# Optimization experiments

Measured on AMD Instinct MI355X. Metric: run time of the kernel, lower is better.

Reference implementation:

```python
import jax, jax.numpy as jnp
import numpy as np

N, E, H, NF, EF = 50000, 1600000, 128, 8, 2


def setup_inputs() -> dict:
    key = jax.random.key(0)
    ks = jax.random.split(key, 24)
    rn = lambda k, shp, s=0.05: jax.random.normal(k, shp, jnp.float32) * s
    inp = {
        "x": jax.random.normal(ks[0], (N, NF), jnp.float32),
        "edge_index": jax.random.randint(ks[1], (2, E), 0, N),
        "edge_attr": jax.random.normal(ks[2], (E, EF), jnp.float32),
        "enc_W": rn(ks[3], (NF, H)),
        "enc_b": jnp.zeros((H,), jnp.float32),
        "bn_g": jnp.ones((H,), jnp.float32),
        "bn_b": jnp.zeros((H,), jnp.float32),
    }
    i = 4
    for l in (1, 2, 3):
        inp[f"W{l}"] = rn(ks[i], (H, H))
        inp[f"asrc{l}"] = rn(ks[i + 1], (H,))
        inp[f"adst{l}"] = rn(ks[i + 2], (H,))
        inp[f"We{l}"] = rn(ks[i + 3], (EF, H))
        inp[f"ae{l}"] = rn(ks[i + 4], (H,))
        inp[f"b{l}"] = jnp.zeros((H,), jnp.float32)
        i += 5
    return inp


def _gat(h, src, dst, ea, W, a_s, a_d, We, a_e, b, n):
    # PyG GATConv, heads=1, concat=True, negative_slope=0.2
    g = h @ W                                   # [N, H] transformed nodes
    a_src = g @ a_s                             # [N] per-source attention term
    a_dst = g @ a_d                             # [N] per-target attention term
    a_edge = (ea @ We) @ a_e                    # [E'] edge-conditioned term
    logit = jax.nn.leaky_relu(a_src[src] + a_dst[dst] + a_edge, negative_slope=0.2)
    # scatter-softmax over incoming edges of each destination node
    m = jax.ops.segment_max(logit, dst, num_segments=n)
    e = jnp.exp(logit - m[dst])
    s = jax.ops.segment_sum(e, dst, num_segments=n)
    alpha = e / (s[dst] + 1e-16)                # [E']
    out = jax.ops.segment_sum(g[src] * alpha[:, None], dst, num_segments=n)
    return out + b


def _forward(x, edge_index, edge_attr, enc_W, enc_b, bn_g, bn_b,
             W1, asrc1, adst1, We1, ae1, b1,
             W2, asrc2, adst2, We2, ae2, b2,
             W3, asrc3, adst3, We3, ae3, b3):
    n = x.shape[0]
    # PyG add_self_loops=True with fill_value='mean' for edge_attr
    loop = jnp.arange(n)
    src = jnp.concatenate([edge_index[0], loop])
    dst = jnp.concatenate([edge_index[1], loop])
    ea = jnp.concatenate([edge_attr, jnp.broadcast_to(edge_attr.mean(0), (n, edge_attr.shape[1]))], axis=0)
    # node encoder: Linear -> BatchNorm1d (eval: running_mean=0, running_var=1) -> ReLU (dropout off)
    inv = np.float32(1.0 / np.sqrt(1.0 + 1e-5))
    h0 = jax.nn.relu((x @ enc_W + enc_b) * (bn_g * inv) + bn_b)
    h1 = jax.nn.relu(_gat(h0, src, dst, ea, W1, asrc1, adst1, We1, ae1, b1, n))
    h2 = jax.nn.relu(_gat(h1, src, dst, ea, W2, asrc2, adst2, We2, ae2, b2, n))
    h3 = _gat(h2, src, dst, ea, W3, asrc3, adst3, We3, ae3, b3, n)
    return h3 + h0


def reference(x, edge_index, edge_attr, enc_W, enc_b, bn_g, bn_b,
              W1, asrc1, adst1, We1, ae1, b1,
              W2, asrc2, adst2, We2, ae2, b2,
              W3, asrc3, adst3, We3, ae3, b3):
    return _forward(x, edge_index, edge_attr, enc_W, enc_b, bn_g, bn_b,
                    W1, asrc1, adst1, We1, ae1, b1,
                    W2, asrc2, adst2, We2, ae2, b2,
                    W3, asrc3, adst3, We3, ae3, b3)
```

## Files before the change

### kernel.cpp

```cpp
#include <hip/hip_runtime.h>
#include <math.h>


#define H 128
#define NF 8
#define EPB 4096

typedef __attribute__((ext_vector_type(8))) short short8v;
typedef __attribute__((ext_vector_type(4))) float f32x4;
typedef __attribute__((ext_vector_type(2))) float f32x2;

__device__ __forceinline__ float wred_sum(float x) {
#pragma unroll
    for (int m = 32; m >= 1; m >>= 1) x += __shfl_xor(x, m, 64);
    return x;
}
__device__ __forceinline__ float wred_max(float x) {
#pragma unroll
    for (int m = 32; m >= 1; m >>= 1) x = fmaxf(x, __shfl_xor(x, m, 64));
    return x;
}
__device__ __forceinline__ ushort f2bf(float f) {
    uint u = __float_as_uint(f);
    uint r = (u + 0x7FFFu + ((u >> 16) & 1u)) >> 16;
    return (ushort)r;
}
__device__ __forceinline__ f32x2 bfpair(uint q) {
    f32x2 r;
    r.x = __uint_as_float(q << 16);
    r.y = __uint_as_float(q & 0xffff0000u);
    return r;
}

__global__ void k_fusedA(const int* __restrict__ ei, const float* __restrict__ ea,
                         int E, int nblk, int nbuckets, int* __restrict__ bucketTotal,
                         int* __restrict__ blockBase, float2* __restrict__ pmean,
                         const float* __restrict__ x, const float* __restrict__ encW,
                         const float* __restrict__ encb, const float* __restrict__ bng,
                         const float* __restrict__ bnb, float* __restrict__ h0,
                         ushort* __restrict__ hb, int N, int GB8,
                         const float* __restrict__ W1, const float* __restrict__ W2,
                         const float* __restrict__ W3, ushort* __restrict__ Wp) {
    __shared__ int hist[256];
    __shared__ float sx[4], sy[4];
    __shared__ float xs[8 * NF];
    const int bx = blockIdx.x;
    const int t = threadIdx.x;

    if (bx < nblk) {
        int blk = bx;
        hist[t] = 0;
        __syncthreads();
        int base = blk * EPB;
        float px = 0.f, py = 0.f;
#pragma unroll
        for (int i = 0; i < 16; ++i) {
            int e = base + i * 256 + t;
            if (e < E) {
                int d = ei[E + e];
                atomicAdd(&hist[d >> 8], 1);
                const float2 z = *(const float2*)(ea + 2 * (size_t)e);
                px += z.x; py += z.y;
            }
        }
        px = wred_sum(px); py = wred_sum(py);
        if ((t & 63) == 0) { sx[t >> 6] = px; sy[t >> 6] = py; }
        __syncthreads();
        if (t == 0) {
            pmean[blk] = make_float2(sx[0] + sx[1] + sx[2] + sx[3],
                                     sy[0] + sy[1] + sy[2] + sy[3]);
        }
        if (t < nbuckets) {
            int c = hist[t];
            int old = (c > 0) ? atomicAdd(&bucketTotal[t], c) : 0;
            blockBase[t * nblk + blk] = old;
        }
    } else if (bx < nblk + GB8) {
        int nb = (bx - nblk) * 8;
        if (t < 64) {
            size_t idx = (size_t)nb * NF + t;
            xs[t] = (idx < (size_t)N * NF) ? x[idx] : 0.f;
        }
        __syncthreads();
        int jt = t & 31, i = t >> 5;
        int node = nb + i;
        int j4 = jt * 4;
        float ax = 0.f, ay = 0.f, az = 0.f, aw = 0.f;
#pragma unroll
        for (int k = 0; k < NF; ++k) {
            float hx = xs[i * NF + k];
            const float4 w = *(const float4*)(encW + k * H + j4);
            ax = fmaf(hx, w.x, ax); ay = fmaf(hx, w.y, ay);
            az = fmaf(hx, w.z, az); aw = fmaf(hx, w.w, aw);
        }
        if (node < N) {
            const float inv = 0.9999950000374997f;
            const float4 eb = *(const float4*)(encb + j4);
            const float4 gg = *(const float4*)(bng + j4);
            const float4 bb = *(const float4*)(bnb + j4);
            float4 o;
            o.x = fmaxf(0.f, (ax + eb.x) * (gg.x * inv) + bb.x);
            o.y = fmaxf(0.f, (ay + eb.y) * (gg.y * inv) + bb.y);
            o.z = fmaxf(0.f, (az + eb.z) * (gg.z * inv) + bb.z);
            o.w = fmaxf(0.f, (aw + eb.w) * (gg.w * inv) + bb.w);
            *(float4*)(h0 + (size_t)node * H + j4) = o;
            uint2 ob;
            ob.x = (uint)f2bf(o.x) | ((uint)f2bf(o.y) << 16);
            ob.y = (uint)f2bf(o.z) | ((uint)f2bf(o.w) << 16);
            *(uint2*)(hb + (size_t)node * H + j4) = ob;
        }
    } else {
        int layer = bx - nblk - GB8;
        const float* W = (layer == 0) ? W1 : ((layer == 1) ? W2 : W3);
        for (int idx = t; idx < 16384; idx += 256) {
            int i = idx & 7;
            int lane = (idx >> 3) & 63;
            int ft = idx >> 9;
            int kt = ft & 3, nt = ft >> 2;
            int k = kt * 32 + (lane >> 4) * 8 + i;
            int n = nt * 16 + (lane & 15);
            Wp[layer * 16384 + idx] = f2bf(W[k * H + n]);
        }
    }
}

__global__ void k_scan_park(const int* __restrict__ bucketTotal, int nbuckets,
                            int* __restrict__ bucketBase, int* __restrict__ rowptr,
                            int N, int E, const float2* __restrict__ pmean, int nblk,
                            float invE,
                            const float* __restrict__ We1, const float* __restrict__ ae1,
                            const float* __restrict__ We2, const float* __restrict__ ae2,
                            const float* __restrict__ We3, const float* __restrict__ ae3,
                            float* __restrict__ park) {
    __shared__ int tmp[256];
    __shared__ float2 sp[4];
    __shared__ float smean[2];
    int t = threadIdx.x;
    float ax = 0.f, ay = 0.f;
    for (int i = t; i < nblk; i += 256) {
        float2 z = pmean[i];
        ax += z.x; ay += z.y;
    }
    ax = wred_sum(ax); ay = wred_sum(ay);
    if ((t & 63) == 0) sp[t >> 6] = make_float2(ax, ay);
    int v = (t < nbuckets) ? bucketTotal[t] : 0;
    tmp[t] = v;
    __syncthreads();
    for (int off = 1; off < 256; off <<= 1) {
        int q = (t >= off) ? tmp[t - off] : 0;
        __syncthreads();
        tmp[t] += q;
        __syncthreads();
    }
    bucketBase[t] = tmp[t] - v;
    if (t == 0) {
        bucketBase[256] = tmp[255];
        rowptr[N] = E;
        smean[0] = (sp[0].x + sp[1].x + sp[2].x + sp[3].x) * invE;
        smean[1] = (sp[0].y + sp[1].y + sp[2].y + sp[3].y) * invE;
    }
    __syncthreads();
    if (t < 192) {
        int l = t >> 6, q = t & 63;
        const float* We = (l == 0) ? We1 : ((l == 1) ? We2 : We3);
        const float* ae = (l == 0) ? ae1 : ((l == 1) ? ae2 : ae3);
        float p0 = We[q] * ae[q] + We[q + 64] * ae[q + 64];
        float p1 = We[H + q] * ae[q] + We[H + q + 64] * ae[q + 64];
        p0 = wred_sum(p0);
        p1 = wred_sum(p1);
        if (q == 0) {
            park[l * 3 + 0] = p0;
            park[l * 3 + 1] = p1;
            park[l * 3 + 2] = smean[0] * p0 + smean[1] * p1;
        }
    }
}

__global__ void k_fusedB(const int* __restrict__ ei, const float* __restrict__ ea,
                         int E, int nblk, int nbuckets,
                         const int* __restrict__ bucketBase, const int* __restrict__ blockBase,
                         uint2* __restrict__ temp,
                         const ushort* __restrict__ hb, const ushort* __restrict__ Wp,
                         const float* __restrict__ avs, const float* __restrict__ avd,
                         ushort* __restrict__ gb, float* __restrict__ a_src,
                         float* __restrict__ a_dst, int N) {
    __shared__ int cnt[256];
    __shared__ int sbase[256];
    __shared__ ushort hs[64 * 136];
    const int tid = threadIdx.x;

    if (blockIdx.x < nblk) {
        int blk = blockIdx.x;
        cnt[tid] = 0;
        if (tid < nbuckets) sbase[tid] = bucketBase[tid] + blockBase[tid * nblk + blk];
        __syncthreads();
        int base = blk * EPB;
#pragma unroll
        for (int i = 0; i < 16; ++i) {
            int e = base + i * 256 + tid;
            if (e < E) {
                int s = ei[e];
                int d = ei[E + e];
                int b = d >> 8;
                int r = atomicAdd(&cnt[b], 1);
                const float2 z = *(const float2*)(ea + 2 * (size_t)e);
                uint w0 = (uint)s | ((uint)(d & 255) << 16);
                uint w1 = (uint)f2bf(z.x) | ((uint)f2bf(z.y) << 16);
                temp[sbase[b] + r] = make_uint2(w0, w1);
            }
        }
        return;
    }

    int nb = (blockIdx.x - nblk) * 64;
#pragma unroll
    for (int it = 0; it < 4; ++it) {
        int fi = it * 256 + tid;
        int r = fi >> 4;
        int c8 = (fi & 15) * 8;
        int node = nb + r;
        uint4 v = make_uint4(0, 0, 0, 0);
        if (node < N) v = *(const uint4*)(hb + (size_t)node * H + c8);
        *(uint4*)(hs + r * 136 + c8) = v;
    }
    __syncthreads();
    const int l = tid & 63;
    const int w = tid >> 6;
    const int cl = l & 15;
    const int kg = l >> 4;
    const ushort* hrow = hs + (w * 16 + cl) * 136 + kg * 8;
    short8v a0 = *(const short8v*)(hrow + 0);
    short8v a1 = *(const short8v*)(hrow + 32);
    short8v a2 = *(const short8v*)(hrow + 64);
    short8v a3 = *(const short8v*)(hrow + 96);

    f32x4 acc[8];
#pragma unroll
    for (int nt = 0; nt < 8; ++nt) {
        const short8v* bp = (const short8v*)(Wp + ((size_t)(nt * 4) * 64 + l) * 8);
        f32x4 c = {0.f, 0.f, 0.f, 0.f};
        c = __builtin_amdgcn_mfma_f32_16x16x32_bf16(a0, bp[0], c, 0, 0, 0);
        c = __builtin_amdgcn_mfma_f32_16x16x32_bf16(a1, bp[64], c, 0, 0, 0);
        c = __builtin_amdgcn_mfma_f32_16x16x32_bf16(a2, bp[128], c, 0, 0, 0);
        c = __builtin_amdgcn_mfma_f32_16x16x32_bf16(a3, bp[192], c, 0, 0, 0);
        acc[nt] = c;
    }

    float ps0 = 0.f, ps1 = 0.f, ps2 = 0.f, ps3 = 0.f;
    float pd0 = 0.f, pd1 = 0.f, pd2 = 0.f, pd3 = 0.f;
#pragma unroll
    for (int nt = 0; nt < 8; ++nt) {
        float vs = avs[cl + 16 * nt];
        float vd = avd[cl + 16 * nt];
        ps0 = fmaf(acc[nt].x, vs, ps0); pd0 = fmaf(acc[nt].x, vd, pd0);
        ps1 = fmaf(acc[nt].y, vs, ps1); pd1 = fmaf(acc[nt].y, vd, pd1);
        ps2 = fmaf(acc[nt].z, vs, ps2); pd2 = fmaf(acc[nt].z, vd, pd2);
        ps3 = fmaf(acc[nt].w, vs, ps3); pd3 = fmaf(acc[nt].w, vd, pd3);
    }
#pragma unroll
    for (int m = 8; m >= 1; m >>= 1) {
        ps0 += __shfl_xor(ps0, m, 64); pd0 += __shfl_xor(pd0, m, 64);
        ps1 += __shfl_xor(ps1, m, 64); pd1 += __shfl_xor(pd1, m, 64);
        ps2 += __shfl_xor(ps2, m, 64); pd2 += __shfl_xor(pd2, m, 64);
        ps3 += __shfl_xor(ps3, m, 64); pd3 += __shfl_xor(pd3, m, 64);
    }
    int r0 = nb + w * 16 + kg * 4;
    if (cl == 0) {
        if (r0 + 0 < N) { a_src[r0 + 0] = ps0; a_dst[r0 + 0] = pd0; }
        if (r0 + 1 < N) { a_src[r0 + 1] = ps1; a_dst[r0 + 1] = pd1; }
        if (r0 + 2 < N) { a_src[r0 + 2] = ps2; a_dst[r0 + 2] = pd2; }
        if (r0 + 3 < N) { a_src[r0 + 3] = ps3; a_dst[r0 + 3] = pd3; }
    }
#pragma unroll
    for (int nt = 0; nt < 8; ++nt) {
        int col = nt * 16 + cl;
        if (r0 + 0 < N) gb[(size_t)(r0 + 0) * H + col] = f2bf(acc[nt].x);
        if (r0 + 1 < N) gb[(size_t)(r0 + 1) * H + col] = f2bf(acc[nt].y);
        if (r0 + 2 < N) gb[(size_t)(r0 + 2) * H + col] = f2bf(acc[nt].z);
        if (r0 + 3 < N) gb[(size_t)(r0 + 3) * H + col] = f2bf(acc[nt].w);
    }
}

__global__ void k_fine(const uint2* __restrict__ temp, const int* __restrict__ bucketBase,
                       const float* __restrict__ park, int N,
                       uint* __restrict__ er0, uint* __restrict__ er1,
                       uint* __restrict__ er2, int* __restrict__ rowptr) {
    __shared__ int hist[256];
    __shared__ int tmp[256];
    __shared__ int fb[256];
    __shared__ int cur[256];
    int b = blockIdx.x;
    int t = threadIdx.x;
    const int lo = bucketBase[b], hi = bucketBase[b + 1];
    hist[t] = 0;
    __syncthreads();
    for (int e = lo + t; e < hi; e += 256) {
        atomicAdd(&hist[(temp[e].x >> 16) & 255], 1);
    }
    __syncthreads();
    int v = hist[t];
    tmp[t] = v;
    __syncthreads();
    for (int off = 1; off < 256; off <<= 1) {
        int q = (t >= off) ? tmp[t - off] : 0;
        __syncthreads();
        tmp[t] += q;
        __syncthreads();
    }
    fb[t] = tmp[t] - v;
    cur[t] = 0;
    int dst = b * 256 + t;
    if (dst < N) rowptr[dst] = lo + fb[t];
    __syncthreads();
    const float c00 = park[0], c01 = park[1];
    const float c10 = park[3], c11 = park[4];
    const float c20 = park[6], c21 = park[7];
    for (int e = lo + t; e < hi; e += 256) {
        uint2 w = temp[e];
        uint src = w.x & 0xFFFFu;
        int j = (int)((w.x >> 16) & 255u);
        float ex = __uint_as_float(w.y << 16);
        float ey = __uint_as_float(w.y & 0xffff0000u);
        int r = atomicAdd(&cur[j], 1);
        int p = lo + fb[j] + r;
        er0[p] = src | ((uint)f2bf(c00 * ex + c01 * ey) << 16);
        er1[p] = src | ((uint)f2bf(c10 * ex + c11 * ey) << 16);
        er2[p] = src | ((uint)f2bf(c20 * ex + c21 * ey) << 16);
    }
}

__global__ void k_gemm_mfma(const ushort* __restrict__ hb, const ushort* __restrict__ Wp,
                            const float* __restrict__ avs, const float* __restrict__ avd,
                            ushort* __restrict__ gb, float* __restrict__ a_src,
                            float* __restrict__ a_dst, int N) {
    __shared__ ushort hs[64 * 136];
    int tid = threadIdx.x;
    int nb = blockIdx.x * 64;
#pragma unroll
    for (int it = 0; it < 4; ++it) {
        int fi = it * 256 + tid;
        int r = fi >> 4;
        int c8 = (fi & 15) * 8;
        int node = nb + r;
        uint4 v = make_uint4(0, 0, 0, 0);
        if (node < N) v = *(const uint4*)(hb + (size_t)node * H + c8);
        *(uint4*)(hs + r * 136 + c8) = v;
    }
    __syncthreads();
    const int l = tid & 63;
    const int w = tid >> 6;
    const int cl = l & 15;
    const int kg = l >> 4;
    const ushort* hrow = hs + (w * 16 + cl) * 136 + kg * 8;
    short8v a0 = *(const short8v*)(hrow + 0);
    short8v a1 = *(const short8v*)(hrow + 32);
    short8v a2 = *(const short8v*)(hrow + 64);
    short8v a3 = *(const short8v*)(hrow + 96);

    f32x4 acc[8];
#pragma unroll
    for (int nt = 0; nt < 8; ++nt) {
        const short8v* bp = (const short8v*)(Wp + ((size_t)(nt * 4) * 64 + l) * 8);
        f32x4 c = {0.f, 0.f, 0.f, 0.f};
        c = __builtin_amdgcn_mfma_f32_16x16x32_bf16(a0, bp[0], c, 0, 0, 0);
        c = __builtin_amdgcn_mfma_f32_16x16x32_bf16(a1, bp[64], c, 0, 0, 0);
        c = __builtin_amdgcn_mfma_f32_16x16x32_bf16(a2, bp[128], c, 0, 0, 0);
        c = __builtin_amdgcn_mfma_f32_16x16x32_bf16(a3, bp[192], c, 0, 0, 0);
        acc[nt] = c;
    }

    float ps0 = 0.f, ps1 = 0.f, ps2 = 0.f, ps3 = 0.f;
    float pd0 = 0.f, pd1 = 0.f, pd2 = 0.f, pd3 = 0.f;
#pragma unroll
    for (int nt = 0; nt < 8; ++nt) {
        float vs = avs[cl + 16 * nt];
        float vd = avd[cl + 16 * nt];
        ps0 = fmaf(acc[nt].x, vs, ps0); pd0 = fmaf(acc[nt].x, vd, pd0);
        ps1 = fmaf(acc[nt].y, vs, ps1); pd1 = fmaf(acc[nt].y, vd, pd1);
        ps2 = fmaf(acc[nt].z, vs, ps2); pd2 = fmaf(acc[nt].z, vd, pd2);
        ps3 = fmaf(acc[nt].w, vs, ps3); pd3 = fmaf(acc[nt].w, vd, pd3);
    }
#pragma unroll
    for (int m = 8; m >= 1; m >>= 1) {
        ps0 += __shfl_xor(ps0, m, 64); pd0 += __shfl_xor(pd0, m, 64);
        ps1 += __shfl_xor(ps1, m, 64); pd1 += __shfl_xor(pd1, m, 64);
        ps2 += __shfl_xor(ps2, m, 64); pd2 += __shfl_xor(pd2, m, 64);
        ps3 += __shfl_xor(ps3, m, 64); pd3 += __shfl_xor(pd3, m, 64);
    }
    int r0 = nb + w * 16 + kg * 4;
    if (cl == 0) {
        if (r0 + 0 < N) { a_src[r0 + 0] = ps0; a_dst[r0 + 0] = pd0; }
        if (r0 + 1 < N) { a_src[r0 + 1] = ps1; a_dst[r0 + 1] = pd1; }
        if (r0 + 2 < N) { a_src[r0 + 2] = ps2; a_dst[r0 + 2] = pd2; }
        if (r0 + 3 < N) { a_src[r0 + 3] = ps3; a_dst[r0 + 3] = pd3; }
    }
#pragma unroll
    for (int nt = 0; nt < 8; ++nt) {
        int col = nt * 16 + cl;
        if (r0 + 0 < N) gb[(size_t)(r0 + 0) * H + col] = f2bf(acc[nt].x);
        if (r0 + 1 < N) gb[(size_t)(r0 + 1) * H + col] = f2bf(acc[nt].y);
        if (r0 + 2 < N) gb[(size_t)(r0 + 2) * H + col] = f2bf(acc[nt].z);
        if (r0 + 3 < N) gb[(size_t)(r0 + 3) * H + col] = f2bf(acc[nt].w);
    }
}

template <int MODE>
__global__ void k_agg(const ushort* __restrict__ gb, const float* __restrict__ a_src,
                      const float* __restrict__ a_dst, const int* __restrict__ rowptr,
                      const uint* __restrict__ erecL, const float* __restrict__ park,
                      int layer, const float* __restrict__ bias,
                      const float* __restrict__ h0, float* __restrict__ outf,
                      ushort* __restrict__ outb, int N) {
    int wv = threadIdx.x >> 6;
    int lane = threadIdx.x & 63;
    int v = blockIdx.x * 4 + wv;
    if (v >= N) return;

    const int grp = lane >> 4;
    const int sub = lane & 15;
    const int ch8 = sub * 8;

    const float sa = park[layer * 3 + 2];
    const float adv = a_dst[v];
    float lself = a_src[v] + adv + sa;
    lself = (lself > 0.f) ? lself : 0.2f * lself;

    float m = lself;
    float s = 1.f;
    f32x2 acc2[4];
    {
        const uint4 q = *(const uint4*)(gb + (size_t)v * H + ch8);
        float sel = (grp == 0) ? 1.f : 0.f;
        acc2[0] = bfpair(q.x) * sel;
        acc2[1] = bfpair(q.y) * sel;
        acc2[2] = bfpair(q.z) * sel;
        acc2[3] = bfpair(q.w) * sel;
    }

    const int rs = rowptr[v];
    const int re = rowptr[v + 1];
    for (int p0 = rs; p0 < re; p0 += 64) {
        int e = p0 + lane;
        bool val = e < re;
        uint rec = val ? __builtin_nontemporal_load(erecL + e) : 0u;
        int sv = (int)(rec & 0xFFFFu);
        float lg;
        if (val) {
            float aef = __uint_as_float(rec & 0xffff0000u);
            lg = a_src[sv] + adv + aef;
            lg = (lg > 0.f) ? lg : 0.2f * lg;
        } else {
            lg = -INFINITY;
        }
        float cm = wred_max(lg);
        float nm = fmaxf(m, cm);
        float f = __expf(m - nm);
        float w = val ? __expf(lg - nm) : 0.f;
        float ws = wred_sum(w);
        s = s * f + ws;
#pragma unroll
        for (int k = 0; k < 4; ++k) acc2[k] *= f;
        m = nm;

        int cnt = re - p0;
        if (cnt > 64) cnt = 64;
        const int cm1 = cnt - 1;
        const int iters = (cnt + 7) >> 3;

        int jA = grp, jB = grp + 4;
        int jAc = (jA <= cm1) ? jA : cm1;
        int jBc = (jB <= cm1) ? jB : cm1;
        float wA = __shfl(w, jAc, 64); if (jA > cm1) wA = 0.f;
        float wB = __shfl(w, jBc, 64); if (jB > cm1) wB = 0.f;
        int sA = __shfl(sv, jAc, 64);
        int sB = __shfl(sv, jBc, 64);
        uint4 qA = *(const uint4*)(gb + (size_t)sA * H + ch8);
        uint4 qB = *(const uint4*)(gb + (size_t)sB * H + ch8);

        for (int i = 0; i < iters; ++i) {
            int jA1 = (i + 1) * 8 + grp, jB1 = jA1 + 4;
            int jA1c = (jA1 <= cm1) ? jA1 : cm1;
            int jB1c = (jB1 <= cm1) ? jB1 : cm1;
            float wA1 = __shfl(w, jA1c, 64); if (jA1 > cm1) wA1 = 0.f;
            float wB1 = __shfl(w, jB1c, 64); if (jB1 > cm1) wB1 = 0.f;
            int sA1 = __shfl(sv, jA1c, 64);
            int sB1 = __shfl(sv, jB1c, 64);
            uint4 qA1 = *(const uint4*)(gb + (size_t)sA1 * H + ch8);
            uint4 qB1 = *(const uint4*)(gb + (size_t)sB1 * H + ch8);

            f32x2 wAv = {wA, wA};
            f32x2 wBv = {wB, wB};
            acc2[0] = __builtin_elementwise_fma(wAv, bfpair(qA.x), acc2[0]);
            acc2[1] = __builtin_elementwise_fma(wAv, bfpair(qA.y), acc2[1]);
            acc2[2] = __builtin_elementwise_fma(wAv, bfpair(qA.z), acc2[2]);
            acc2[3] = __builtin_elementwise_fma(wAv, bfpair(qA.w), acc2[3]);
            acc2[0] = __builtin_elementwise_fma(wBv, bfpair(qB.x), acc2[0]);
            acc2[1] = __builtin_elementwise_fma(wBv, bfpair(qB.y), acc2[1]);
            acc2[2] = __builtin_elementwise_fma(wBv, bfpair(qB.z), acc2[2]);
            acc2[3] = __builtin_elementwise_fma(wBv, bfpair(qB.w), acc2[3]);

            wA = wA1; wB = wB1; qA = qA1; qB = qB1;
        }
    }

    float acc[8];
    acc[0] = acc2[0].x; acc[1] = acc2[0].y;
    acc[2] = acc2[1].x; acc[3] = acc2[1].y;
    acc[4] = acc2[2].x; acc[5] = acc2[2].y;
    acc[6] = acc2[3].x; acc[7] = acc2[3].y;
#pragma unroll
    for (int k = 0; k < 8; ++k) {
        acc[k] += __shfl_xor(acc[k], 16, 64);
        acc[k] += __shfl_xor(acc[k], 32, 64);
    }

    if (grp == 0) {
        const float is = 1.f / s;
        const float4 b0 = *(const float4*)(bias + ch8);
        const float4 b1 = *(const float4*)(bias + ch8 + 4);
        float o[8];
        o[0] = acc[0] * is + b0.x; o[1] = acc[1] * is + b0.y;
        o[2] = acc[2] * is + b0.z; o[3] = acc[3] * is + b0.w;
        o[4] = acc[4] * is + b1.x; o[5] = acc[5] * is + b1.y;
        o[6] = acc[6] * is + b1.z; o[7] = acc[7] * is + b1.w;
        if (MODE == 0) {
#pragma unroll
            for (int k = 0; k < 8; ++k) o[k] = fmaxf(o[k], 0.f);
            uint4 ob;
            ob.x = (uint)f2bf(o[0]) | ((uint)f2bf(o[1]) << 16);
            ob.y = (uint)f2bf(o[2]) | ((uint)f2bf(o[3]) << 16);
            ob.z = (uint)f2bf(o[4]) | ((uint)f2bf(o[5]) << 16);
            ob.w = (uint)f2bf(o[6]) | ((uint)f2bf(o[7]) << 16);
            *(uint4*)(outb + (size_t)v * H + ch8) = ob;
        } else {
            const float4 ha = *(const float4*)(h0 + (size_t)v * H + ch8);
            const float4 hb4 = *(const float4*)(h0 + (size_t)v * H + ch8 + 4);
            o[0] += ha.x; o[1] += ha.y; o[2] += ha.z; o[3] += ha.w;
            o[4] += hb4.x; o[5] += hb4.y; o[6] += hb4.z; o[7] += hb4.w;
            *(float4*)(outf + (size_t)v * H + ch8) = make_float4(o[0], o[1], o[2], o[3]);
            *(float4*)(outf + (size_t)v * H + ch8 + 4) = make_float4(o[4], o[5], o[6], o[7]);
        }
    }
}


extern "C" void kernel_launch(void* const* d_in, const int* in_sizes, int n_in,
                              void* d_out, int out_size, void* d_ws, size_t ws_size,
                              hipStream_t stream) {
    const float* x    = (const float*)d_in[0];
    const int*   ei   = (const int*)d_in[1];
    const float* ea   = (const float*)d_in[2];
    const float* encW = (const float*)d_in[3];
    const float* encb = (const float*)d_in[4];
    const float* bng  = (const float*)d_in[5];
    const float* bnb  = (const float*)d_in[6];
    const float *W[3], *asrc[3], *adst[3], *We[3], *aev[3], *bias[3];
    for (int l = 0; l < 3; ++l) {
        W[l]    = (const float*)d_in[7 + l * 6 + 0];
        asrc[l] = (const float*)d_in[7 + l * 6 + 1];
        adst[l] = (const float*)d_in[7 + l * 6 + 2];
        We[l]   = (const float*)d_in[7 + l * 6 + 3];
        aev[l]  = (const float*)d_in[7 + l * 6 + 4];
        bias[l] = (const float*)d_in[7 + l * 6 + 5];
    }
    const int N = in_sizes[0] / NF;
    const int E = in_sizes[1] / 2;
    float* out = (float*)d_out;

    const int NBu  = (N + 255) >> 8;
    const int nblk = (E + EPB - 1) / EPB;
    const int GB8  = (N + 7) / 8;
    const int GBM  = (N + 63) / 64;
    const int AB   = (N + 3) / 4;

    char* wp = (char*)d_ws;
    auto alloc = [&](size_t bytes) -> char* {
        char* p = wp;
        wp += (bytes + 255) & ~(size_t)255;
        return p;
    };
    float*  h0       = (float*)alloc((size_t)N * H * 4);
    ushort* hb       = (ushort*)alloc((size_t)N * H * 2);
    ushort* gb       = (ushort*)alloc((size_t)N * H * 2);
    ushort* Wp       = (ushort*)alloc((size_t)3 * 16384 * 2);
    float*  a_src    = (float*)alloc((size_t)N * 4);
    float*  a_dst    = (float*)alloc((size_t)N * 4);
    int*    rowptr   = (int*)alloc((size_t)(N + 1) * 4);
    float*  park     = (float*)alloc(64);
    int*    bucketTotal = (int*)alloc(256 * 4);
    int*    bucketBase  = (int*)alloc(257 * 4);
    int*    blockBase   = (int*)alloc((size_t)NBu * nblk * 4);
    uint*   er0      = (uint*)alloc((size_t)E * 4);
    uint*   er1      = (uint*)alloc((size_t)E * 4);
    uint*   er2      = (uint*)alloc((size_t)E * 4);
    float2* pmean    = (float2*)alloc((size_t)nblk * 8);
    uint2*  temp     = (uint2*)alloc((size_t)E * 8);

    hipMemsetAsync(bucketTotal, 0, 256 * 4, stream);

    k_fusedA<<<nblk + GB8 + 3, 256, 0, stream>>>(
        ei, ea, E, nblk, NBu, bucketTotal, blockBase, pmean,
        x, encW, encb, bng, bnb, h0, hb, N, GB8,
        W[0], W[1], W[2], Wp);
    k_scan_park<<<1, 256, 0, stream>>>(bucketTotal, NBu, bucketBase, rowptr, N, E,
                                       pmean, nblk, 1.0f / (float)E,
                                       We[0], aev[0], We[1], aev[1], We[2], aev[2], park);
    k_fusedB<<<nblk + GBM, 256, 0, stream>>>(
        ei, ea, E, nblk, NBu, bucketBase, blockBase, temp,
        hb, Wp + 0 * 16384, asrc[0], adst[0], gb, a_src, a_dst, N);
    k_fine<<<NBu, 256, 0, stream>>>(temp, bucketBase, park, N, er0, er1, er2, rowptr);

    k_agg<0><<<AB, 256, 0, stream>>>(gb, a_src, a_dst, rowptr, er0, park, 0,
                                     bias[0], nullptr, nullptr, hb, N);
    k_gemm_mfma<<<GBM, 256, 0, stream>>>(hb, Wp + 1 * 16384, asrc[1], adst[1],
                                         gb, a_src, a_dst, N);
    k_agg<0><<<AB, 256, 0, stream>>>(gb, a_src, a_dst, rowptr, er1, park, 1,
                                     bias[1], nullptr, nullptr, hb, N);
    k_gemm_mfma<<<GBM, 256, 0, stream>>>(hb, Wp + 2 * 16384, asrc[2], adst[2],
                                         gb, a_src, a_dst, N);
    k_agg<1><<<AB, 256, 0, stream>>>(gb, a_src, a_dst, rowptr, er2, park, 2,
                                     bias[2], h0, out, nullptr, N);
}
```

Measured before the change: 298.8 us.

## Split aggregation into softmax-stats pass and channel-sliced gather pass

Replaces the single online-softmax aggregation kernel with two kernels: one computes each node's max and inverse softmax sum, and the other gathers neighbor features with exact weights. The gather is split into four 32-channel slices across separate blocks, with 16 edges handled in parallel per wave instead of 4 software-pipelined pairs. This removes the per-chunk rescaling and is meant to raise memory-level parallelism and occupancy in the gather. In exchange, the edge records, a_src lookups and exponentials are recomputed in both kernels and four times across the slices, and three extra launches are added.

```diff
diff --git a/kernel.cpp b/kernel.cpp
--- a/kernel.cpp
+++ b/kernel.cpp
@@ -8,7 +8,6 @@
 
 typedef __attribute__((ext_vector_type(8))) short short8v;
 typedef __attribute__((ext_vector_type(4))) float f32x4;
-typedef __attribute__((ext_vector_type(2))) float f32x2;
 
 __device__ __forceinline__ float wred_sum(float x) {
 #pragma unroll
@@ -25,12 +24,8 @@
     uint r = (u + 0x7FFFu + ((u >> 16) & 1u)) >> 16;
     return (ushort)r;
 }
-__device__ __forceinline__ f32x2 bfpair(uint q) {
-    f32x2 r;
-    r.x = __uint_as_float(q << 16);
-    r.y = __uint_as_float(q & 0xffff0000u);
-    return r;
-}
+__device__ __forceinline__ float bflo(uint q) { return __uint_as_float(q << 16); }
+__device__ __forceinline__ float bfhi(uint q) { return __uint_as_float(q & 0xffff0000u); }
 
 __global__ void k_fusedA(const int* __restrict__ ei, const float* __restrict__ ea,
                          int E, int nblk, int nbuckets, int* __restrict__ bucketTotal,
@@ -404,22 +399,15 @@
     }
 }
 
-template <int MODE>
-__global__ void k_agg(const ushort* __restrict__ gb, const float* __restrict__ a_src,
-                      const float* __restrict__ a_dst, const int* __restrict__ rowptr,
-                      const uint* __restrict__ erecL, const float* __restrict__ park,
-                      int layer, const float* __restrict__ bias,
-                      const float* __restrict__ h0, float* __restrict__ outf,
-                      ushort* __restrict__ outb, int N) {
+__global__ void k_soft(const float* __restrict__ a_src, const float* __restrict__ a_dst,
+                       const int* __restrict__ rowptr, const uint* __restrict__ erecL,
+                       const float* __restrict__ park, int layer,
+                       float* __restrict__ sm, float* __restrict__ sis, int N) {
     int wv = threadIdx.x >> 6;
     int lane = threadIdx.x & 63;
     int v = blockIdx.x * 4 + wv;
     if (v >= N) return;
 
-    const int grp = lane >> 4;
-    const int sub = lane & 15;
-    const int ch8 = sub * 8;
-
     const float sa = park[layer * 3 + 2];
     const float adv = a_dst[v];
     float lself = a_src[v] + adv + sa;
@@ -427,16 +415,6 @@
 
     float m = lself;
     float s = 1.f;
-    f32x2 acc2[4];
-    {
-        const uint4 q = *(const uint4*)(gb + (size_t)v * H + ch8);
-        float sel = (grp == 0) ? 1.f : 0.f;
-        acc2[0] = bfpair(q.x) * sel;
-        acc2[1] = bfpair(q.y) * sel;
-        acc2[2] = bfpair(q.z) * sel;
-        acc2[3] = bfpair(q.w) * sel;
-    }
-
     const int rs = rowptr[v];
     const int re = rowptr[v + 1];
     for (int p0 = rs; p0 < re; p0 += 64) {
@@ -458,64 +436,109 @@
         float w = val ? __expf(lg - nm) : 0.f;
         float ws = wred_sum(w);
         s = s * f + ws;
-#pragma unroll
-        for (int k = 0; k < 4; ++k) acc2[k] *= f;
         m = nm;
-
+    }
+    if (lane == 0) {
+        sm[v] = m;
+        sis[v] = 1.f / s;
+    }
+}
+
+template <int MODE>
+__global__ void k_gath(const ushort* __restrict__ gb, const float* __restrict__ a_src,
+                       const float* __restrict__ a_dst, const int* __restrict__ rowptr,
+                       const uint* __restrict__ erecL, const float* __restrict__ park,
+                       int layer, const float* __restrict__ sm, const float* __restrict__ sis,
+                       const float* __restrict__ bias, const float* __restrict__ h0,
+                       float* __restrict__ outf, ushort* __restrict__ outb, int N) {
+    const int sl = blockIdx.x & 3;
+    const int wv = threadIdx.x >> 6;
+    const int lane = threadIdx.x & 63;
+    const int v = (blockIdx.x >> 2) * 4 + wv;
+    if (v >= N) return;
+
+    const int grp = lane >> 2;
+    const int sub = lane & 3;
+    const int ch8 = sl * 32 + sub * 8;
+
+    const float sa = park[layer * 3 + 2];
+    const float adv = a_dst[v];
+    const float mv = sm[v];
+    float lself = a_src[v] + adv + sa;
+    lself = (lself > 0.f) ? lself : 0.2f * lself;
+    const float wself = __expf(lself - mv);
+
+    float acc[8];
+    {
+        const uint4 q = *(const uint4*)(gb + (size_t)v * H + ch8);
+        float sel = (grp == 0) ? wself : 0.f;
+        acc[0] = sel * bflo(q.x); acc[1] = sel * bfhi(q.x);
+        acc[2] = sel * bflo(q.y); acc[3] = sel * bfhi(q.y);
+        acc[4] = sel * bflo(q.z); acc[5] = sel * bfhi(q.z);
+        acc[6] = sel * bflo(q.w); acc[7] = sel * bfhi(q.w);
+    }
+
+#define ACC8(W, Q)                                     \
+    acc[0] = fmaf(W, bflo(Q.x), acc[0]);               \
+    acc[1] = fmaf(W, bfhi(Q.x), acc[1]);               \
+    acc[2] = fmaf(W, bflo(Q.y), acc[2]);               \
+    acc[3] = fmaf(W, bfhi(Q.y), acc[3]);               \
+    acc[4] = fmaf(W, bflo(Q.z), acc[4]);               \
+    acc[5] = fmaf(W, bfhi(Q.z), acc[5]);               \
+    acc[6] = fmaf(W, bflo(Q.w), acc[6]);               \
+    acc[7] = fmaf(W, bfhi(Q.w), acc[7]);
+
+    const int rs = rowptr[v];
+    const int re = rowptr[v + 1];
+    for (int p0 = rs; p0 < re; p0 += 64) {
+        int e = p0 + lane;
+        bool val = e < re;
+        uint rec = val ? __builtin_nontemporal_load(erecL + e) : 0u;
+        int sv = (int)(rec & 0xFFFFu);
+        float w = 0.f;
+        if (val) {
+            float aef = __uint_as_float(rec & 0xffff0000u);
+            float lg = a_src[sv] + adv + aef;
+            lg = (lg > 0.f) ? lg : 0.2f * lg;
+            w = __expf(lg - mv);
+        }
         int cnt = re - p0;
         if (cnt > 64) cnt = 64;
         const int cm1 = cnt - 1;
-        const int iters = (cnt + 7) >> 3;
-
-        int jA = grp, jB = grp + 4;
-        int jAc = (jA <= cm1) ? jA : cm1;
-        int jBc = (jB <= cm1) ? jB : cm1;
-        float wA = __shfl(w, jAc, 64); if (jA > cm1) wA = 0.f;
-        float wB = __shfl(w, jBc, 64); if (jB > cm1) wB = 0.f;
-        int sA = __shfl(sv, jAc, 64);
-        int sB = __shfl(sv, jBc, 64);
-        uint4 qA = *(const uint4*)(gb + (size_t)sA * H + ch8);
-        uint4 qB = *(const uint4*)(gb + (size_t)sB * H + ch8);
-
-        for (int i = 0; i < iters; ++i) {
-            int jA1 = (i + 1) * 8 + grp, jB1 = jA1 + 4;
-            int jA1c = (jA1 <= cm1) ? jA1 : cm1;
-            int jB1c = (jB1 <= cm1) ? jB1 : cm1;
-            float wA1 = __shfl(w, jA1c, 64); if (jA1 > cm1) wA1 = 0.f;
-            float wB1 = __shfl(w, jB1c, 64); if (jB1 > cm1) wB1 = 0.f;
-            int sA1 = __shfl(sv, jA1c, 64);
-            int sB1 = __shfl(sv, jB1c, 64);
-            uint4 qA1 = *(const uint4*)(gb + (size_t)sA1 * H + ch8);
-            uint4 qB1 = *(const uint4*)(gb + (size_t)sB1 * H + ch8);
-
-            f32x2 wAv = {wA, wA};
-            f32x2 wBv = {wB, wB};
-            acc2[0] = __builtin_elementwise_fma(wAv, bfpair(qA.x), acc2[0]);
-            acc2[1] = __builtin_elementwise_fma(wAv, bfpair(qA.y), acc2[1]);
-            acc2[2] = __builtin_elementwise_fma(wAv, bfpair(qA.z), acc2[2]);
-            acc2[3] = __builtin_elementwise_fma(wAv, bfpair(qA.w), acc2[3]);
-            acc2[0] = __builtin_elementwise_fma(wBv, bfpair(qB.x), acc2[0]);
-            acc2[1] = __builtin_elementwise_fma(wBv, bfpair(qB.y), acc2[1]);
-            acc2[2] = __builtin_elementwise_fma(wBv, bfpair(qB.z), acc2[2]);
-            acc2[3] = __builtin_elementwise_fma(wBv, bfpair(qB.w), acc2[3]);
-
-            wA = wA1; wB = wB1; qA = qA1; qB = qB1;
-        }
-    }
-
-    float acc[8];
-    acc[0] = acc2[0].x; acc[1] = acc2[0].y;
-    acc[2] = acc2[1].x; acc[3] = acc2[1].y;
-    acc[4] = acc2[2].x; acc[5] = acc2[2].y;
-    acc[6] = acc2[3].x; acc[7] = acc2[3].y;
+
+        int j0 = grp,      j0c = (j0 <= cm1) ? j0 : cm1;
+        int j1 = grp + 16, j1c = (j1 <= cm1) ? j1 : cm1;
+        int j2 = grp + 32, j2c = (j2 <= cm1) ? j2 : cm1;
+        int j3 = grp + 48, j3c = (j3 <= cm1) ? j3 : cm1;
+        float w0 = __shfl(w, j0c, 64); if (j0 > cm1) w0 = 0.f;
+        float w1 = __shfl(w, j1c, 64); if (j1 > cm1) w1 = 0.f;
+        float w2 = __shfl(w, j2c, 64); if (j2 > cm1) w2 = 0.f;
+        float w3 = __shfl(w, j3c, 64); if (j3 > cm1) w3 = 0.f;
+        int s0 = __shfl(sv, j0c, 64);
+        int s1 = __shfl(sv, j1c, 64);
+        int s2 = __shfl(sv, j2c, 64);
+        int s3 = __shfl(sv, j3c, 64);
+        const uint4 q0 = *(const uint4*)(gb + (size_t)s0 * H + ch8);
+        const uint4 q1 = *(const uint4*)(gb + (size_t)s1 * H + ch8);
+        const uint4 q2 = *(const uint4*)(gb + (size_t)s2 * H + ch8);
+        const uint4 q3 = *(const uint4*)(gb + (size_t)s3 * H + ch8);
+        ACC8(w0, q0);
+        ACC8(w1, q1);
+        ACC8(w2, q2);
+        ACC8(w3, q3);
+    }
+#undef ACC8
+
 #pragma unroll
     for (int k = 0; k < 8; ++k) {
+        acc[k] += __shfl_xor(acc[k], 4, 64);
+        acc[k] += __shfl_xor(acc[k], 8, 64);
         acc[k] += __shfl_xor(acc[k], 16, 64);
         acc[k] += __shfl_xor(acc[k], 32, 64);
     }
 
     if (grp == 0) {
-        const float is = 1.f / s;
+        const float is = sis[v];
         const float4 b0 = *(const float4*)(bias + ch8);
         const float4 b1 = *(const float4*)(bias + ch8 + 4);
         float o[8];
@@ -572,6 +595,7 @@
     const int GB8  = (N + 7) / 8;
     const int GBM  = (N + 63) / 64;
     const int AB   = (N + 3) / 4;
+    const int AB4  = AB * 4;
 
     char* wp = (char*)d_ws;
     auto alloc = [&](size_t bytes) -> char* {
@@ -585,6 +609,8 @@
     ushort* Wp       = (ushort*)alloc((size_t)3 * 16384 * 2);
     float*  a_src    = (float*)alloc((size_t)N * 4);
     float*  a_dst    = (float*)alloc((size_t)N * 4);
+    float*  sm       = (float*)alloc((size_t)N * 4);
+    float*  sis      = (float*)alloc((size_t)N * 4);
     int*    rowptr   = (int*)alloc((size_t)(N + 1) * 4);
     float*  park     = (float*)alloc(64);
     int*    bucketTotal = (int*)alloc(256 * 4);
@@ -610,14 +636,17 @@
         hb, Wp + 0 * 16384, asrc[0], adst[0], gb, a_src, a_dst, N);
     k_fine<<<NBu, 256, 0, stream>>>(temp, bucketBase, park, N, er0, er1, er2, rowptr);
 
-    k_agg<0><<<AB, 256, 0, stream>>>(gb, a_src, a_dst, rowptr, er0, park, 0,
-                                     bias[0], nullptr, nullptr, hb, N);
+    k_soft<<<AB, 256, 0, stream>>>(a_src, a_dst, rowptr, er0, park, 0, sm, sis, N);
+    k_gath<0><<<AB4, 256, 0, stream>>>(gb, a_src, a_dst, rowptr, er0, park, 0,
+                                       sm, sis, bias[0], nullptr, nullptr, hb, N);
     k_gemm_mfma<<<GBM, 256, 0, stream>>>(hb, Wp + 1 * 16384, asrc[1], adst[1],
                                          gb, a_src, a_dst, N);
-    k_agg<0><<<AB, 256, 0, stream>>>(gb, a_src, a_dst, rowptr, er1, park, 1,
-                                     bias[1], nullptr, nullptr, hb, N);
+    k_soft<<<AB, 256, 0, stream>>>(a_src, a_dst, rowptr, er1, park, 1, sm, sis, N);
+    k_gath<0><<<AB4, 256, 0, stream>>>(gb, a_src, a_dst, rowptr, er1, park, 1,
+                                       sm, sis, bias[1], nullptr, nullptr, hb, N);
     k_gemm_mfma<<<GBM, 256, 0, stream>>>(hb, Wp + 2 * 16384, asrc[2], adst[2],
                                          gb, a_src, a_dst, N);
-    k_agg<1><<<AB, 256, 0, stream>>>(gb, a_src, a_dst, rowptr, er2, park, 2,
-                                     bias[2], h0, out, nullptr, N);
-}
+    k_soft<<<AB, 256, 0, stream>>>(a_src, a_dst, rowptr, er2, park, 2, sm, sis, N);
+    k_gath<1><<<AB4, 256, 0, stream>>>(gb, a_src, a_dst, rowptr, er2, park, 2,
+                                       sm, sis, bias[2], h0, out, nullptr, N);
+}
```

Result: slower. 527.1 us (+76.4%).
